# Kernel optimization log

Hardware: AMD Instinct MI355X
Metric: run time of the kernel (lower is better)

## Reference

```python
import jax, jax.numpy as jnp
import numpy as np

D_MODEL = 1024
D_INNER = 1024
N_HEADS = 16
D_HEAD = D_INNER // N_HEADS
B = 2
CUR = 1024
PREV = 1024
LN_EPS = 1e-5


def _rel_shift(x):
    # x: (b, i, j, h) -- faithful to torch: pad along i, flat-reinterpret, drop first row
    b, i, j, h = x.shape
    zp = jnp.zeros((b, 1, j, h), x.dtype)
    xp = jnp.concatenate([zp, x], axis=1).reshape(i + 1, b, j, h)
    return xp[1:].reshape(b, i, j, h)


def setup_inputs() -> dict:
    key = jax.random.key(0)
    ks = jax.random.split(key, 10)
    x = jax.random.normal(ks[0], (B, CUR, D_MODEL), jnp.float32)
    mem = jax.random.normal(ks[1], (B, PREV, D_MODEL), jnp.float32)
    pos_emb = jax.random.normal(ks[2], (CUR + PREV, D_INNER), jnp.float32)
    u = jax.random.normal(ks[3], (N_HEADS, D_HEAD), jnp.float32) * 0.02
    v = jax.random.normal(ks[4], (N_HEADS, D_HEAD), jnp.float32) * 0.02
    # causal mask: query i (current segment) may attend key j if j <= i + PREV
    idx_i = jnp.arange(CUR)[:, None]
    idx_j = jnp.arange(CUR + PREV)[None, :]
    tgt_mask = jnp.broadcast_to((idx_j > idx_i + PREV)[None, :, :, None], (B, CUR, CUR + PREV, 1))
    Wq = jax.random.normal(ks[5], (D_INNER, D_MODEL), jnp.float32) * 0.02
    Wkv = jax.random.normal(ks[6], (2 * D_INNER, D_MODEL), jnp.float32) * 0.02
    Wfc = jax.random.normal(ks[7], (D_MODEL, D_INNER), jnp.float32) * 0.02
    bfc = jnp.zeros((D_MODEL,), jnp.float32)
    gamma = jnp.ones((D_MODEL,), jnp.float32)
    beta = jnp.zeros((D_MODEL,), jnp.float32)
    return {"x": x, "pos_emb": pos_emb, "u": u, "v": v, "mem": mem,
            "tgt_mask": tgt_mask, "Wq": Wq, "Wkv": Wkv, "Wfc": Wfc,
            "bfc": bfc, "gamma": gamma, "beta": beta}


def reference(x, pos_emb, u, v, mem, tgt_mask, Wq, Wkv, Wfc, bfc, gamma, beta):
    b, cur, _ = x.shape
    prev = mem.shape[1]
    tot = cur + prev
    h_telda = jnp.concatenate([mem, x], axis=1)               # (b, tot, d_model)
    q = jnp.einsum('bsm,im->bsi', x, Wq)                      # (b, cur, d_inner)
    kv = jnp.einsum('bsm,im->bsi', h_telda, Wkv)              # (b, tot, 2*d_inner)
    k, vv = kv[..., :D_INNER], kv[..., D_INNER:]
    q = q.reshape(b, cur, N_HEADS, D_HEAD)
    k = k.reshape(b, tot, N_HEADS, D_HEAD)
    vv = vv.reshape(b, tot, N_HEADS, D_HEAD)
    content = jnp.einsum('bihd,bjhd->bijh', q + u, k)
    pos = pos_emb.reshape(tot, N_HEADS, D_HEAD)
    pos_attn = jnp.einsum('bihd,jhd->bijh', q + v, pos)
    attn = content + _rel_shift(pos_attn)
    attn = jnp.where(tgt_mask, -jnp.inf, attn)
    attn = attn / (D_HEAD ** 0.5)
    attn = jax.nn.softmax(attn, axis=1)  # faithful: softmax over query dim as in original
    out = jnp.einsum('bijh,bjhd->bihd', attn, vv).reshape(b, cur, D_INNER)
    y = x + jnp.einsum('bsi,mi->bsm', out, Wfc) + bfc
    mu = jnp.mean(y, axis=-1, keepdims=True)
    var = jnp.mean((y - mu) ** 2, axis=-1, keepdims=True)
    return (y - mu) / jnp.sqrt(var + LN_EPS) * gamma + beta
```

## Files before the change

kernel.cpp:

```cpp
#include <hip/hip_runtime.h>
#include <hip/hip_bf16.h>
#include <stdint.h>

typedef unsigned short u16;
typedef __attribute__((ext_vector_type(8))) __bf16 bf16x8;
typedef __attribute__((ext_vector_type(4))) float f32x4;
typedef __attribute__((ext_vector_type(4))) float float4v;
typedef __attribute__((ext_vector_type(4))) u16  u16x4;
typedef __attribute__((ext_vector_type(8))) u16  u16x8;

#define DEV __device__ __forceinline__

#define NB   2
#define CUR  1024
#define PREV 1024
#define TOT  2048
#define DM   1024
#define NH   16
#define DH   64

DEV u16 f2b(float f) {
    uint32_t u = __builtin_bit_cast(uint32_t, f);
    uint32_t r = (u + 0x7fffu + ((u >> 16) & 1u)) >> 16;
    return (u16)r;
}
DEV float b2f(u16 u) {
    return __builtin_bit_cast(float, (uint32_t)u << 16);
}

typedef const __attribute__((address_space(1))) void* gptr_t;
typedef __attribute__((address_space(3))) void*       lptr_t;
DEV void async16(const void* g, void* l) {
    __builtin_amdgcn_global_load_lds((gptr_t)g, (lptr_t)l, 16, 0, 0);
}

template<int BM, int BN, int BK, int WM, int WN, int EPI>
__global__ __launch_bounds__(256)
void gemm_bt(const u16* __restrict__ A, const u16* __restrict__ B,
             int M, int N, int K, long sA, long sB, int bzBase,
             void* __restrict__ C0, void* __restrict__ C1,
             const float* __restrict__ F0, const float* __restrict__ F1)
{
    constexpr int WAVES_N = BN / WN;
    constexpr int MI = WM / 16, NI = WN / 16;
    static_assert((BM / WM) * (BN / WN) == 4, "4 waves");
    static_assert((BM * BK) % 2048 == 0 && (BN * BK) % 2048 == 0, "staging");

    __shared__ u16 lA[BM * BK];
    __shared__ u16 lB[BN * BK];

    const int bz  = blockIdx.z;
    const int m0 = blockIdx.y * BM, n0 = blockIdx.x * BN;
    const int tid = threadIdx.x, wave = tid >> 6, lane = tid & 63;

    if constexpr (EPI == 3) {
        if (n0 > m0 + BM - 1 + PREV) {
            u16* Cz = (u16*)C0 + (long)bz * M * (long)N;
            u16x8 z8 = {};
#pragma unroll
            for (int e = tid * 8; e < BM * BN; e += 2048) {
                int r = e / BN, cc = e % BN;
                *(u16x8*)(Cz + (long)(m0 + r) * N + n0 + cc) = z8;
            }
            return;
        }
    }

    const u16* Ab = A + (long)bz * sA;
    const u16* Bb = B + (long)bz * sB;
    const int wm0 = (wave / WAVES_N) * WM, wn0 = (wave % WAVES_N) * WN;

    f32x4 acc[MI][NI];
#pragma unroll
    for (int mi = 0; mi < MI; ++mi)
#pragma unroll
        for (int ni = 0; ni < NI; ++ni)
            acc[mi][ni] = f32x4{0.f, 0.f, 0.f, 0.f};

    int Kend = K;
    if constexpr (EPI == 4) {
        int t = m0 + BM + PREV;
        Kend = t < K ? t : K;
    }

    for (int kt = 0; kt < Kend; kt += BK) {
        __syncthreads();
#pragma unroll
        for (int is = 0; is < (BM * BK) / 2048; ++is) {
            int e = is * 2048 + tid * 8;
            int r = e / BK, k = e % BK;
            async16(Ab + (long)(m0 + r) * K + kt + k, &lA[is * 2048 + wave * 512]);
        }
#pragma unroll
        for (int is = 0; is < (BN * BK) / 2048; ++is) {
            int e = is * 2048 + tid * 8;
            int r = e / BK, k = e % BK;
            async16(Bb + (long)(n0 + r) * K + kt + k, &lB[is * 2048 + wave * 512]);
        }
        __syncthreads();
#pragma unroll
        for (int ks = 0; ks < BK; ks += 32) {
            bf16x8 af[MI], br[NI];
#pragma unroll
            for (int mi = 0; mi < MI; ++mi)
                af[mi] = *(const bf16x8*)(const void*)&lA[(wm0 + mi * 16 + (lane & 15)) * BK + ks + ((lane >> 4) * 8)];
#pragma unroll
            for (int ni = 0; ni < NI; ++ni)
                br[ni] = *(const bf16x8*)(const void*)&lB[(wn0 + ni * 16 + (lane & 15)) * BK + ks + ((lane >> 4) * 8)];
#pragma unroll
            for (int mi = 0; mi < MI; ++mi)
#pragma unroll
                for (int ni = 0; ni < NI; ++ni)
                    acc[mi][ni] = __builtin_amdgcn_mfma_f32_16x16x32_bf16(af[mi], br[ni], acc[mi][ni], 0, 0, 0);
        }
    }

    const int gbz = bzBase + bz;
#pragma unroll
    for (int ni = 0; ni < NI; ++ni) {
        const int n = n0 + wn0 + ni * 16 + (lane & 15);
        float csum = 0.f;
#pragma unroll
        for (int mi = 0; mi < MI; ++mi) {
#pragma unroll
            for (int r = 0; r < 4; ++r) {
                const int m = m0 + wm0 + mi * 16 + ((lane >> 4) << 2) + r;
                float c = acc[mi][ni][r];
                if constexpr (EPI == 1) {
                    int b = gbz, i = m, h = n >> 6, d = n & 63;
                    u16* Abuf = (u16*)C0;
                    Abuf[(((long)(b * NH + h)) * CUR + i) * 128 + d] = f2b(c + F0[n]);
                    float qv = c + F1[n];
                    if (b == 0) {
                        if (i > 0)     Abuf[(((long)h) * CUR + (i - 1)) * 128 + 64 + d] = f2b(qv);
                        if (i == 1023) Abuf[(((long)h) * CUR + 1023) * 128 + 64 + d] = 0;
                    } else {
                        Abuf[(((long)(NH + h)) * CUR + i) * 128 + 64 + d] = f2b(qv);
                    }
                } else if constexpr (EPI == 2) {
                    int b = m >> 11, j = m & 2047;
                    if (n < DM) {
                        int h = n >> 6, d = n & 63;
                        ((u16*)C0)[(((long)(b * NH + h)) * TOT + j) * 128 + d] = f2b(c);
                    } else {
                        int h = (n - DM) >> 6, d = n & 63;
                        ((u16*)C1)[(((long)(b * NH + h)) * TOT + j) * 64 + d] = f2b(c);
                    }
                } else if constexpr (EPI == 3) {
                    float e = (n > m + PREV) ? 0.f : __expf(c * 0.125f);
                    ((u16*)C0)[((long)bz * M + m) * (long)N + n] = f2b(e);
                    csum += e;
                } else if constexpr (EPI == 4) {
                    int b = gbz >> 4, h = gbz & 15;
                    ((u16*)C0)[((long)b * CUR + m) * DM + h * DH + n] = f2b(c);
                } else if constexpr (EPI == 5) {
                    ((float*)C0)[(long)m * DM + n] = F0[(long)m * DM + n] + c + F1[n];
                }
            }
        }
        if constexpr (EPI == 3) {
            csum += __shfl_xor(csum, 16);
            csum += __shfl_xor(csum, 32);
            if ((lane >> 4) == 0)
                atomicAdd(((float*)C1) + (long)gbz * TOT + n, csum);
        }
    }
}

__global__ __launch_bounds__(256)
void cvt_bf16(const float* __restrict__ src, u16* __restrict__ dst, int n4)
{
    int i = blockIdx.x * 256 + threadIdx.x;
    if (i < n4) {
        float4v f = ((const float4v*)src)[i];
        u16x4 o = {f2b(f[0]), f2b(f[1]), f2b(f[2]), f2b(f[3])};
        ((u16x4*)dst)[i] = o;
    }
}

__global__ __launch_bounds__(256)
void pack_H(const float* __restrict__ mem, const float* __restrict__ x, u16* __restrict__ dst)
{
    int i = blockIdx.x * 256 + threadIdx.x;
    int e = i << 2;
    int b = e >> 21, r = e & ((1 << 21) - 1);
    const float* src = (r < (1 << 20)) ? (mem + ((long)b << 20) + r)
                                       : (x + ((long)b << 20) + (r - (1 << 20)));
    float4v f = *(const float4v*)src;
    u16x4 o = {f2b(f[0]), f2b(f[1]), f2b(f[2]), f2b(f[3])};
    ((u16x4*)dst)[i] = o;
}

__global__ __launch_bounds__(256)
void pack_pos(const float* __restrict__ pos, u16* __restrict__ Bbuf)
{
    int i = blockIdx.x * 256 + threadIdx.x;
    int e = i << 2;
    int h = e >> 17, r = e & 131071, j = r >> 6, d = r & 63;
    float4v f = *(const float4v*)(pos + (long)j * DM + h * DH + d);
    u16x4 o = {f2b(f[0]), f2b(f[1]), f2b(f[2]), f2b(f[3])};
    long base = ((long)h * TOT + j) * 128 + 64 + d;
    *(u16x4*)(Bbuf + base) = o;
    *(u16x4*)(Bbuf + base + (long)NH * TOT * 128) = o;
}

__global__ __launch_bounds__(256)
void vprime_kernel(const u16* __restrict__ Vtmp, const float* __restrict__ colsum,
                   u16* __restrict__ Vp, int bzBase)
{
    __shared__ float t[64][65];
    int bz = bzBase + blockIdx.y;
    int j0 = blockIdx.x * 64;
    const u16* src = Vtmp + ((long)bz * TOT + j0) * 64;
    const float* cs = colsum + (long)bz * TOT + j0;
    for (int e = threadIdx.x; e < 4096; e += 256) {
        int jl = e >> 6, d = e & 63;
        t[jl][d] = b2f(src[e]) / cs[jl];
    }
    __syncthreads();
    u16* dst = Vp + (long)bz * DH * TOT + j0;
    for (int e = threadIdx.x; e < 4096; e += 256) {
        int d = e >> 6, jl = e & 63;
        dst[(long)d * TOT + jl] = f2b(t[jl][d]);
    }
}

__global__ __launch_bounds__(256)
void ln_kernel(const float* __restrict__ Y, const float* __restrict__ gamma,
               const float* __restrict__ beta, float* __restrict__ out)
{
    const int row = blockIdx.x;
    const float* y = Y + (long)row * DM;
    float v[4];
    float s = 0.f;
#pragma unroll
    for (int t = 0; t < 4; ++t) { v[t] = y[threadIdx.x + t * 256]; s += v[t]; }
#pragma unroll
    for (int off = 32; off > 0; off >>= 1) s += __shfl_down(s, off);
    __shared__ float r1[4], r2[4];
    int wv = threadIdx.x >> 6, ln = threadIdx.x & 63;
    if (ln == 0) r1[wv] = s;
    __syncthreads();
    float mu = (r1[0] + r1[1] + r1[2] + r1[3]) * (1.f / DM);
    float q = 0.f;
#pragma unroll
    for (int t = 0; t < 4; ++t) { float d = v[t] - mu; q += d * d; }
#pragma unroll
    for (int off = 32; off > 0; off >>= 1) q += __shfl_down(q, off);
    if (ln == 0) r2[wv] = q;
    __syncthreads();
    float var = (r2[0] + r2[1] + r2[2] + r2[3]) * (1.f / DM);
    float inv = rsqrtf(var + 1e-5f);
#pragma unroll
    for (int t = 0; t < 4; ++t) {
        int c = threadIdx.x + t * 256;
        out[(long)row * DM + c] = (v[t] - mu) * inv * gamma[c] + beta[c];
    }
}

extern "C" void kernel_launch(void* const* d_in, const int* in_sizes, int n_in,
                              void* d_out, int out_size, void* d_ws, size_t ws_size,
                              hipStream_t stream)
{
    const float* x     = (const float*)d_in[0];
    const float* pos   = (const float*)d_in[1];
    const float* u     = (const float*)d_in[2];
    const float* vbias = (const float*)d_in[3];
    const float* mem   = (const float*)d_in[4];
    const float* Wq    = (const float*)d_in[6];
    const float* Wkv   = (const float*)d_in[7];
    const float* Wfc   = (const float*)d_in[8];
    const float* bfc   = (const float*)d_in[9];
    const float* gamma = (const float*)d_in[10];
    const float* beta  = (const float*)d_in[11];
    float* out = (float*)d_out;

    char* w = (char*)d_ws;
    auto alloc = [&](size_t bytes) {
        char* p = w;
        w += (bytes + 255) & ~(size_t)255;
        return p;
    };
    u16*   Hb     = (u16*)alloc(4096UL * 1024 * 2);
    u16*   Wqb    = (u16*)alloc(1024UL * 1024 * 2);
    u16*   Wkvb   = (u16*)alloc(2048UL * 1024 * 2);
    u16*   Wfcb   = (u16*)alloc(1024UL * 1024 * 2);
    u16*   Abuf   = (u16*)alloc(32UL * 1024 * 128 * 2);
    u16*   Bbuf   = (u16*)alloc(32UL * 2048 * 128 * 2);
    u16*   Vtmp   = (u16*)alloc(32UL * 2048 * 64 * 2);
    u16*   Vp     = (u16*)alloc(32UL * 64 * 2048 * 2);
    float* colsum = (float*)alloc(32UL * 2048 * 4);
    u16*   Obf    = (u16*)alloc(2048UL * 1024 * 2);
    float* Yf     = (float*)alloc(2048UL * 1024 * 4);
    u16*   Ebuf   = (u16*)alloc(32UL * 1024 * 2048 * 2);

    hipMemsetAsync(colsum, 0, 32UL * 2048 * 4, stream);

    cvt_bf16<<<1024, 256, 0, stream>>>(Wq,  Wqb,  1024 * 1024 / 4);
    cvt_bf16<<<2048, 256, 0, stream>>>(Wkv, Wkvb, 2048 * 1024 / 4);
    cvt_bf16<<<1024, 256, 0, stream>>>(Wfc, Wfcb, 1024 * 1024 / 4);
    pack_H  <<<4096, 256, 0, stream>>>(mem, x, Hb);
    pack_pos<<<2048, 256, 0, stream>>>(pos, Bbuf);

    gemm_bt<128, 128, 64, 64, 64, 1><<<dim3(8, 8, 2), 256, 0, stream>>>(
        Hb + 1024UL * 1024, Wqb, 1024, 1024, 1024, 2048L * 1024, 0, 0,
        Abuf, nullptr, u, vbias);
    gemm_bt<128, 128, 64, 64, 64, 2><<<dim3(16, 32, 1), 256, 0, stream>>>(
        Hb, Wkvb, 4096, 2048, 1024, 0, 0, 0, Bbuf, Vtmp, nullptr, nullptr);

    gemm_bt<128, 128, 64, 64, 64, 3><<<dim3(16, 8, 32), 256, 0, stream>>>(
        Abuf, Bbuf, 1024, 2048, 128, 1024L * 128, 2048L * 128, 0,
        Ebuf, colsum, nullptr, nullptr);
    vprime_kernel<<<dim3(32, 32), 256, 0, stream>>>(Vtmp, colsum, Vp, 0);
    gemm_bt<64, 64, 64, 32, 32, 4><<<dim3(1, 16, 32), 256, 0, stream>>>(
        Ebuf, Vp, 1024, 64, 2048, 1024L * 2048, 64L * 2048, 0,
        Obf, nullptr, nullptr, nullptr);

    gemm_bt<128, 128, 64, 64, 64, 5><<<dim3(8, 16, 1), 256, 0, stream>>>(
        Obf, Wfcb, 2048, 1024, 1024, 0, 0, 0, Yf, nullptr, x, bfc);
    ln_kernel<<<2048, 256, 0, stream>>>(Yf, gamma, beta, out);
}
```

Baseline: 204.9 us.

## Swap GEMM operands for vectorized epilogue stores, XOR-swizzle LDS, fuse weight casts

Every GEMM now computes the transposed product by swapping A and B, so each lane's four accumulator rows fall on contiguous output columns. The epilogues can then write packed 4-element bf16/float vectors instead of scattered scalar stores. The LDS staging and fragment reads use an XOR swizzle on the 16-byte chunk index to cut bank conflicts. The three weight conversion launches are merged into one kernel, and the causal-masked E tiles are skipped outright instead of being zero-filled. The change relies on the swapped layouts matching downstream consumers, and it leaves the skipped E tiles unwritten, which the downstream Kend limit has to cover.

```diff
diff --git a/kernel.cpp b/kernel.cpp
--- a/kernel.cpp
+++ b/kernel.cpp
@@ -7,7 +7,6 @@
 typedef __attribute__((ext_vector_type(4))) float f32x4;
 typedef __attribute__((ext_vector_type(4))) float float4v;
 typedef __attribute__((ext_vector_type(4))) u16  u16x4;
-typedef __attribute__((ext_vector_type(8))) u16  u16x8;
 
 #define DEV __device__ __forceinline__
 
@@ -44,31 +43,24 @@
     constexpr int WAVES_N = BN / WN;
     constexpr int MI = WM / 16, NI = WN / 16;
     static_assert((BM / WM) * (BN / WN) == 4, "4 waves");
+    static_assert(BK == 64, "swizzle assumes 8 chunks/row");
     static_assert((BM * BK) % 2048 == 0 && (BN * BK) % 2048 == 0, "staging");
 
     __shared__ u16 lA[BM * BK];
     __shared__ u16 lB[BN * BK];
 
-    const int bz  = blockIdx.z;
+    const int bz = blockIdx.z;
     const int m0 = blockIdx.y * BM, n0 = blockIdx.x * BN;
     const int tid = threadIdx.x, wave = tid >> 6, lane = tid & 63;
 
     if constexpr (EPI == 3) {
-        if (n0 > m0 + BM - 1 + PREV) {
-            u16* Cz = (u16*)C0 + (long)bz * M * (long)N;
-            u16x8 z8 = {};
-#pragma unroll
-            for (int e = tid * 8; e < BM * BN; e += 2048) {
-                int r = e / BN, cc = e % BN;
-                *(u16x8*)(Cz + (long)(m0 + r) * N + n0 + cc) = z8;
-            }
-            return;
-        }
+        if (m0 > n0 + BN - 1 + PREV) return;
     }
 
     const u16* Ab = A + (long)bz * sA;
     const u16* Bb = B + (long)bz * sB;
     const int wm0 = (wave / WAVES_N) * WM, wn0 = (wave % WAVES_N) * WN;
+    const int quad = lane >> 4;
 
     f32x4 acc[MI][NI];
 #pragma unroll
@@ -79,23 +71,24 @@
 
     int Kend = K;
     if constexpr (EPI == 4) {
-        int t = m0 + BM + PREV;
+        int t = n0 + BN + PREV;
         Kend = t < K ? t : K;
     }
+
+    const int srow = tid >> 3;
+    const int ksw  = (((tid & 7) ^ ((tid >> 3) & 7)) << 3);
 
     for (int kt = 0; kt < Kend; kt += BK) {
         __syncthreads();
 #pragma unroll
         for (int is = 0; is < (BM * BK) / 2048; ++is) {
-            int e = is * 2048 + tid * 8;
-            int r = e / BK, k = e % BK;
-            async16(Ab + (long)(m0 + r) * K + kt + k, &lA[is * 2048 + wave * 512]);
+            int r = is * 32 + srow;
+            async16(Ab + (long)(m0 + r) * K + kt + ksw, &lA[is * 2048 + wave * 512]);
         }
 #pragma unroll
         for (int is = 0; is < (BN * BK) / 2048; ++is) {
-            int e = is * 2048 + tid * 8;
-            int r = e / BK, k = e % BK;
-            async16(Bb + (long)(n0 + r) * K + kt + k, &lB[is * 2048 + wave * 512]);
+            int r = is * 32 + srow;
+            async16(Bb + (long)(n0 + r) * K + kt + ksw, &lB[is * 2048 + wave * 512]);
         }
         __syncthreads();
 #pragma unroll
@@ -103,10 +96,14 @@
             bf16x8 af[MI], br[NI];
 #pragma unroll
             for (int mi = 0; mi < MI; ++mi)
-                af[mi] = *(const bf16x8*)(const void*)&lA[(wm0 + mi * 16 + (lane & 15)) * BK + ks + ((lane >> 4) * 8)];
+                af[mi] = *(const bf16x8*)(const void*)
+                    &lA[(wm0 + mi * 16 + (lane & 15)) * BK +
+                        ((((ks >> 3) + quad) ^ (lane & 7)) << 3)];
 #pragma unroll
             for (int ni = 0; ni < NI; ++ni)
-                br[ni] = *(const bf16x8*)(const void*)&lB[(wn0 + ni * 16 + (lane & 15)) * BK + ks + ((lane >> 4) * 8)];
+                br[ni] = *(const bf16x8*)(const void*)
+                    &lB[(wn0 + ni * 16 + (lane & 15)) * BK +
+                        ((((ks >> 3) + quad) ^ (lane & 7)) << 3)];
 #pragma unroll
             for (int mi = 0; mi < MI; ++mi)
 #pragma unroll
@@ -116,66 +113,139 @@
     }
 
     const int gbz = bzBase + bz;
-#pragma unroll
-    for (int ni = 0; ni < NI; ++ni) {
-        const int n = n0 + wn0 + ni * 16 + (lane & 15);
-        float csum = 0.f;
-#pragma unroll
-        for (int mi = 0; mi < MI; ++mi) {
+
+    if constexpr (EPI == 1) {
+        u16* Abuf = (u16*)C0;
+        const int b = gbz;
+#pragma unroll
+        for (int mi = 0; mi < MI; ++mi) {
+            const int m = m0 + wm0 + mi * 16 + quad * 4;
+            const int h = m >> 6, d = m & 63;
+            const float4v uu = *(const float4v*)(F0 + m);
+            const float4v vv = *(const float4v*)(F1 + m);
+#pragma unroll
+            for (int ni = 0; ni < NI; ++ni) {
+                const int i = n0 + wn0 + ni * 16 + (lane & 15);
+                u16x4 pu, pv;
+#pragma unroll
+                for (int r = 0; r < 4; ++r) {
+                    pu[r] = f2b(acc[mi][ni][r] + uu[r]);
+                    pv[r] = f2b(acc[mi][ni][r] + vv[r]);
+                }
+                *(u16x4*)(Abuf + (((long)(b * NH + h)) * CUR + i) * 128 + d) = pu;
+                if (b == 0) {
+                    if (i > 0)
+                        *(u16x4*)(Abuf + (((long)h) * CUR + (i - 1)) * 128 + 64 + d) = pv;
+                    if (i == 1023) {
+                        u16x4 z = {};
+                        *(u16x4*)(Abuf + (((long)h) * CUR + 1023) * 128 + 64 + d) = z;
+                    }
+                } else {
+                    *(u16x4*)(Abuf + (((long)(NH + h)) * CUR + i) * 128 + 64 + d) = pv;
+                }
+            }
+        }
+    } else if constexpr (EPI == 2) {
+#pragma unroll
+        for (int mi = 0; mi < MI; ++mi) {
+            const int m = m0 + wm0 + mi * 16 + quad * 4;
+            const bool isV = m >= DM;
+            const int h = (m >> 6) & 15, d = m & 63;
+#pragma unroll
+            for (int ni = 0; ni < NI; ++ni) {
+                const int n = n0 + wn0 + ni * 16 + (lane & 15);
+                const int b = n >> 11, j = n & 2047;
+                u16x4 p;
+#pragma unroll
+                for (int r = 0; r < 4; ++r) p[r] = f2b(acc[mi][ni][r]);
+                if (!isV)
+                    *(u16x4*)((u16*)C0 + (((long)(b * NH + h)) * TOT + j) * 128 + d) = p;
+                else
+                    *(u16x4*)((u16*)C1 + (((long)(b * NH + h)) * TOT + j) * 64 + d) = p;
+            }
+        }
+    } else if constexpr (EPI == 3) {
+        u16* Eb = (u16*)C0 + (long)gbz * ((long)CUR * TOT);
+        float ps[MI][4];
+#pragma unroll
+        for (int mi = 0; mi < MI; ++mi)
+#pragma unroll
+            for (int r = 0; r < 4; ++r) ps[mi][r] = 0.f;
+#pragma unroll
+        for (int mi = 0; mi < MI; ++mi) {
+            const int m = m0 + wm0 + mi * 16 + quad * 4;
+#pragma unroll
+            for (int ni = 0; ni < NI; ++ni) {
+                const int n = n0 + wn0 + ni * 16 + (lane & 15);
+                u16x4 p;
+#pragma unroll
+                for (int r = 0; r < 4; ++r) {
+                    float e = (m + r > n + PREV) ? 0.f : __expf(acc[mi][ni][r] * 0.125f);
+                    p[r] = f2b(e);
+                    ps[mi][r] += e;
+                }
+                *(u16x4*)(Eb + (long)n * TOT + m) = p;
+            }
+        }
+        float* CS = (float*)C1 + (long)gbz * TOT;
+#pragma unroll
+        for (int mi = 0; mi < MI; ++mi)
 #pragma unroll
             for (int r = 0; r < 4; ++r) {
-                const int m = m0 + wm0 + mi * 16 + ((lane >> 4) << 2) + r;
-                float c = acc[mi][ni][r];
-                if constexpr (EPI == 1) {
-                    int b = gbz, i = m, h = n >> 6, d = n & 63;
-                    u16* Abuf = (u16*)C0;
-                    Abuf[(((long)(b * NH + h)) * CUR + i) * 128 + d] = f2b(c + F0[n]);
-                    float qv = c + F1[n];
-                    if (b == 0) {
-                        if (i > 0)     Abuf[(((long)h) * CUR + (i - 1)) * 128 + 64 + d] = f2b(qv);
-                        if (i == 1023) Abuf[(((long)h) * CUR + 1023) * 128 + 64 + d] = 0;
-                    } else {
-                        Abuf[(((long)(NH + h)) * CUR + i) * 128 + 64 + d] = f2b(qv);
-                    }
-                } else if constexpr (EPI == 2) {
-                    int b = m >> 11, j = m & 2047;
-                    if (n < DM) {
-                        int h = n >> 6, d = n & 63;
-                        ((u16*)C0)[(((long)(b * NH + h)) * TOT + j) * 128 + d] = f2b(c);
-                    } else {
-                        int h = (n - DM) >> 6, d = n & 63;
-                        ((u16*)C1)[(((long)(b * NH + h)) * TOT + j) * 64 + d] = f2b(c);
-                    }
-                } else if constexpr (EPI == 3) {
-                    float e = (n > m + PREV) ? 0.f : __expf(c * 0.125f);
-                    ((u16*)C0)[((long)bz * M + m) * (long)N + n] = f2b(e);
-                    csum += e;
-                } else if constexpr (EPI == 4) {
-                    int b = gbz >> 4, h = gbz & 15;
-                    ((u16*)C0)[((long)b * CUR + m) * DM + h * DH + n] = f2b(c);
-                } else if constexpr (EPI == 5) {
-                    ((float*)C0)[(long)m * DM + n] = F0[(long)m * DM + n] + c + F1[n];
-                }
-            }
-        }
-        if constexpr (EPI == 3) {
-            csum += __shfl_xor(csum, 16);
-            csum += __shfl_xor(csum, 32);
-            if ((lane >> 4) == 0)
-                atomicAdd(((float*)C1) + (long)gbz * TOT + n, csum);
-        }
-    }
-}
-
-__global__ __launch_bounds__(256)
-void cvt_bf16(const float* __restrict__ src, u16* __restrict__ dst, int n4)
+                float vv = ps[mi][r];
+                vv += __shfl_xor(vv, 1);
+                vv += __shfl_xor(vv, 2);
+                vv += __shfl_xor(vv, 4);
+                vv += __shfl_xor(vv, 8);
+                if ((lane & 15) == 0)
+                    atomicAdd(CS + m0 + wm0 + mi * 16 + quad * 4 + r, vv);
+            }
+    } else if constexpr (EPI == 4) {
+        const int b = gbz >> 4, h = gbz & 15;
+        u16* Ob = (u16*)C0 + (long)b * CUR * DM + h * DH;
+#pragma unroll
+        for (int mi = 0; mi < MI; ++mi) {
+            const int m = m0 + wm0 + mi * 16 + quad * 4;
+#pragma unroll
+            for (int ni = 0; ni < NI; ++ni) {
+                const int n = n0 + wn0 + ni * 16 + (lane & 15);
+                u16x4 p;
+#pragma unroll
+                for (int r = 0; r < 4; ++r) p[r] = f2b(acc[mi][ni][r]);
+                *(u16x4*)(Ob + (long)n * DM + m) = p;
+            }
+        }
+    } else if constexpr (EPI == 5) {
+#pragma unroll
+        for (int mi = 0; mi < MI; ++mi) {
+            const int m = m0 + wm0 + mi * 16 + quad * 4;
+            const float4v bb = *(const float4v*)(F1 + m);
+#pragma unroll
+            for (int ni = 0; ni < NI; ++ni) {
+                const int n = n0 + wn0 + ni * 16 + (lane & 15);
+                const float4v xr = *(const float4v*)(F0 + (long)n * DM + m);
+                float4v y;
+#pragma unroll
+                for (int r = 0; r < 4; ++r) y[r] = xr[r] + acc[mi][ni][r] + bb[r];
+                *(float4v*)((float*)C0 + (long)n * DM + m) = y;
+            }
+        }
+    }
+}
+
+__global__ __launch_bounds__(256)
+void cvt_weights(const float* __restrict__ Wq, const float* __restrict__ Wkv,
+                 const float* __restrict__ Wfc, u16* __restrict__ Wqb,
+                 u16* __restrict__ Wkvb, u16* __restrict__ Wfcb)
 {
     int i = blockIdx.x * 256 + threadIdx.x;
-    if (i < n4) {
-        float4v f = ((const float4v*)src)[i];
-        u16x4 o = {f2b(f[0]), f2b(f[1]), f2b(f[2]), f2b(f[3])};
-        ((u16x4*)dst)[i] = o;
-    }
+    const float* s; u16* d; int off;
+    if (i < 262144)      { s = Wq;  d = Wqb;  off = i; }
+    else if (i < 786432) { s = Wkv; d = Wkvb; off = i - 262144; }
+    else                 { s = Wfc; d = Wfcb; off = i - 786432; }
+    float4v f = ((const float4v*)s)[off];
+    u16x4 o = {f2b(f[0]), f2b(f[1]), f2b(f[2]), f2b(f[3])};
+    ((u16x4*)d)[off] = o;
 }
 
 __global__ __launch_bounds__(256)
@@ -296,27 +366,25 @@
 
     hipMemsetAsync(colsum, 0, 32UL * 2048 * 4, stream);
 
-    cvt_bf16<<<1024, 256, 0, stream>>>(Wq,  Wqb,  1024 * 1024 / 4);
-    cvt_bf16<<<2048, 256, 0, stream>>>(Wkv, Wkvb, 2048 * 1024 / 4);
-    cvt_bf16<<<1024, 256, 0, stream>>>(Wfc, Wfcb, 1024 * 1024 / 4);
+    cvt_weights<<<4096, 256, 0, stream>>>(Wq, Wkv, Wfc, Wqb, Wkvb, Wfcb);
     pack_H  <<<4096, 256, 0, stream>>>(mem, x, Hb);
     pack_pos<<<2048, 256, 0, stream>>>(pos, Bbuf);
 
-    gemm_bt<128, 128, 64, 64, 64, 1><<<dim3(8, 8, 2), 256, 0, stream>>>(
-        Hb + 1024UL * 1024, Wqb, 1024, 1024, 1024, 2048L * 1024, 0, 0,
+    gemm_bt<128, 64, 64, 64, 32, 1><<<dim3(16, 8, 2), 256, 0, stream>>>(
+        Wqb, Hb + 1024UL * 1024, 1024, 1024, 1024, 0, 2048L * 1024, 0,
         Abuf, nullptr, u, vbias);
-    gemm_bt<128, 128, 64, 64, 64, 2><<<dim3(16, 32, 1), 256, 0, stream>>>(
-        Hb, Wkvb, 4096, 2048, 1024, 0, 0, 0, Bbuf, Vtmp, nullptr, nullptr);
-
-    gemm_bt<128, 128, 64, 64, 64, 3><<<dim3(16, 8, 32), 256, 0, stream>>>(
-        Abuf, Bbuf, 1024, 2048, 128, 1024L * 128, 2048L * 128, 0,
+    gemm_bt<128, 128, 64, 64, 64, 2><<<dim3(32, 16, 1), 256, 0, stream>>>(
+        Wkvb, Hb, 2048, 4096, 1024, 0, 0, 0, Bbuf, Vtmp, nullptr, nullptr);
+
+    gemm_bt<128, 128, 64, 64, 64, 3><<<dim3(8, 16, 32), 256, 0, stream>>>(
+        Bbuf, Abuf, 2048, 1024, 128, 2048L * 128, 1024L * 128, 0,
         Ebuf, colsum, nullptr, nullptr);
     vprime_kernel<<<dim3(32, 32), 256, 0, stream>>>(Vtmp, colsum, Vp, 0);
-    gemm_bt<64, 64, 64, 32, 32, 4><<<dim3(1, 16, 32), 256, 0, stream>>>(
-        Ebuf, Vp, 1024, 64, 2048, 1024L * 2048, 64L * 2048, 0,
+    gemm_bt<64, 64, 64, 32, 32, 4><<<dim3(16, 1, 32), 256, 0, stream>>>(
+        Vp, Ebuf, 64, 1024, 2048, 64L * 2048, 1024L * 2048, 0,
         Obf, nullptr, nullptr, nullptr);
 
-    gemm_bt<128, 128, 64, 64, 64, 5><<<dim3(8, 16, 1), 256, 0, stream>>>(
-        Obf, Wfcb, 2048, 1024, 1024, 0, 0, 0, Yf, nullptr, x, bfc);
+    gemm_bt<64, 128, 64, 32, 64, 5><<<dim3(16, 16, 1), 256, 0, stream>>>(
+        Wfcb, Obf, 1024, 2048, 1024, 0, 0, 0, Yf, nullptr, x, bfc);
     ln_kernel<<<2048, 256, 0, stream>>>(Yf, gamma, beta, out);
 }
```

Measured after the change: 185.2 us. -9.6%, faster.
